# Kernel tuning notes

Measured on AMD Instinct MI355X. Metric: run time of the kernel, lower is better.

## Reference

```python
import jax, jax.numpy as jnp
import numpy as np

N = 100000      # nodes
E = 1600000     # edges
F_IN = 128      # num_features
H = 64          # hidden_channels
EPS = 1e-5      # batchnorm eps


def _bn(x, gamma, beta, mean, var):
    # inference-mode BatchNorm1d
    return (x - mean) * jax.lax.rsqrt(var + EPS) * gamma + beta


def setup_inputs() -> dict:
    key = jax.random.key(0)
    ks = jax.random.split(key, 16)

    def lin_w(k, fan_in, fan_out):
        return (jax.random.normal(k, (fan_in, fan_out), jnp.float32)
                * (1.0 / np.sqrt(fan_in)))

    return {
        "x": jax.random.normal(ks[0], (N, F_IN), jnp.float32),
        "edge_index": jax.random.randint(ks[1], (2, E), 0, N, dtype=jnp.int32),
        # node_encoder: Linear(F_IN,H) + BN
        "enc_W": lin_w(ks[2], F_IN, H), "enc_b": jnp.zeros((H,), jnp.float32),
        "enc_g": jnp.ones((H,), jnp.float32), "enc_beta": jnp.zeros((H,), jnp.float32),
        "enc_mean": jnp.zeros((H,), jnp.float32), "enc_var": jnp.ones((H,), jnp.float32),
        # GCNConv layers (PyG: lin without bias, bias added after aggregation)
        "conv1_W": lin_w(ks[3], H, H), "conv1_b": jnp.zeros((H,), jnp.float32),
        "conv2_W": lin_w(ks[4], H, H), "conv2_b": jnp.zeros((H,), jnp.float32),
        # edge_predictor: Linear(2H,H) + BN + Linear(H,1)
        "ep1_W": lin_w(ks[5], 2 * H, H), "ep1_b": jnp.zeros((H,), jnp.float32),
        "ep_g": jnp.ones((H,), jnp.float32), "ep_beta": jnp.zeros((H,), jnp.float32),
        "ep_mean": jnp.zeros((H,), jnp.float32), "ep_var": jnp.ones((H,), jnp.float32),
        "ep2_W": lin_w(ks[6], H, 1), "ep2_b": jnp.zeros((1,), jnp.float32),
    }


def reference(x, edge_index, enc_W, enc_b, enc_g, enc_beta, enc_mean, enc_var,
              conv1_W, conv1_b, conv2_W, conv2_b,
              ep1_W, ep1_b, ep_g, ep_beta, ep_mean, ep_var, ep2_W, ep2_b):
    row, col = edge_index[0], edge_index[1]

    # GCN normalization with added self-loops (symmetric D^-1/2 (A+I) D^-1/2)
    loops = jnp.arange(N, dtype=row.dtype)
    row_sl = jnp.concatenate([row, loops])          # [E+N]
    col_sl = jnp.concatenate([col, loops])
    deg = jax.ops.segment_sum(jnp.ones_like(col_sl, jnp.float32), col_sl, N)
    dinv = jnp.where(deg > 0, jax.lax.rsqrt(jnp.maximum(deg, 1.0)), 0.0)
    norm = dinv[row_sl] * dinv[col_sl]              # [E+N]

    def gcn_conv(h, W, b):
        hw = h @ W                                   # [N,H]
        msg = hw[row_sl] * norm[:, None]             # gather-scale  [E+N,H]
        return jax.ops.segment_sum(msg, col_sl, N) + b  # scatter-add

    # node encoder (inference: dropout = identity)
    h = jax.nn.relu(_bn(x @ enc_W + enc_b, enc_g, enc_beta, enc_mean, enc_var))
    h = jax.nn.relu(gcn_conv(h, conv1_W, conv1_b))
    h = jax.nn.relu(gcn_conv(h, conv2_W, conv2_b))
    node_embeddings = h

    # edge predictor: gather + cat + MLP + sigmoid
    ef = jnp.concatenate([h[row], h[col]], axis=1)   # [E, 2H]
    e = jax.nn.relu(_bn(ef @ ep1_W + ep1_b, ep_g, ep_beta, ep_mean, ep_var))
    edge_pred = jax.nn.sigmoid(e @ ep2_W + ep2_b)    # [E, 1]
    return node_embeddings, edge_pred
```

## Files before the change

### kernel.cpp

```cpp
#include <hip/hip_runtime.h>
#include <hip/hip_bf16.h>
#include <hip/hip_fp16.h>

#define NN 100000
#define NE 1600000
#define FIN 128
#define HD 64
#define NB_MF 1563
#define BSH 8
#define BUCK 256
#define NBUCK 392
#define BCAP 5120
#define CHUNK 4096
#define NCHUNK 391
#define ESPLIT 2
#define NEB (NBUCK*ESPLIT)
#define NFB 6250
#define NAGG 6250

typedef unsigned int uint32;
typedef _Float16 half8 __attribute__((ext_vector_type(8)));
typedef float f32x4 __attribute__((ext_vector_type(4)));
typedef float f32x8 __attribute__((ext_vector_type(8)));

__global__ void __launch_bounds__(256) k_prep(const float* __restrict__ encW, const float* __restrict__ c1W,
                                              const float* __restrict__ c2W, const float* __restrict__ ep1W,
                                              _Float16* __restrict__ wt,
                                              const float* __restrict__ encB, const float* __restrict__ encG,
                                              const float* __restrict__ encBe, const float* __restrict__ encM,
                                              const float* __restrict__ encV,
                                              const float* __restrict__ ep1b, const float* __restrict__ epG,
                                              const float* __restrict__ epBe, const float* __restrict__ epM,
                                              const float* __restrict__ epV,
                                              float* __restrict__ foldEnc, float* __restrict__ foldPre,
                                              int* __restrict__ bcnt, _Float16* __restrict__ bufBzero){
    int blk = blockIdx.x, t = threadIdx.x;
    if(blk < 96){
        int i = blk*256 + t;
        if(i < 8192){
            int n = i >> 7, k = i & 127;
            wt[i] = (_Float16)encW[k*64 + n];
        } else if(i < 12288){
            int j = i - 8192; int n = j >> 6, k = j & 63;
            wt[i] = (_Float16)c1W[k*64 + n];
        } else if(i < 16384){
            int j = i - 12288; int n = j >> 6, k = j & 63;
            wt[i] = (_Float16)c2W[k*64 + n];
        } else {
            int j = i - 16384; int h = j >> 12; int jj = j & 4095;
            int n = jj >> 6, k = jj & 63;
            wt[i] = (_Float16)ep1W[(h*64 + k)*64 + n];
        }
    } else {
        if(t < 64){
            int j = t;
            float s = encG[j]*rsqrtf(encV[j]+1e-5f);
            foldEnc[j]      = s;
            foldEnc[64+j]   = (encB[j]-encM[j])*s + encBe[j];
            float sp = epG[j]*rsqrtf(epV[j]+1e-5f);
            foldPre[j]      = sp;
            foldPre[64+j]   = sp;
            foldPre[128+j]  = sp*(ep1b[j]-epM[j]) + epBe[j];
            foldPre[192+j]  = 0.f;
            bufBzero[j]     = (_Float16)0.f;
        }
        for(int i = t; i < NBUCK; i += 256) bcnt[i] = 0;
    }
}

__global__ void __launch_bounds__(256) k_part(const int* __restrict__ row,
                                              const int* __restrict__ col,
                                              int* __restrict__ bcnt,
                                              uint32* __restrict__ staged,
                                              uint32* __restrict__ posE){
    __shared__ int h[512];
    __shared__ int sc[512];
    __shared__ int gb[512];
    __shared__ uint32 lcsr[CHUNK];
    __shared__ int dst[CHUNK];
    int t = threadIdx.x;
    int e0 = blockIdx.x * CHUNK;
    int e1 = min(e0 + CHUNK, NE);
    h[t] = 0; h[256+t] = 0;
    __syncthreads();
    for(int e = e0 + t; e < e1; e += 256)
        atomicAdd(&h[col[e] >> BSH], 1);
    __syncthreads();
    int c0 = h[t], c1 = h[256+t];
    int i2 = 256 + t;
    gb[t]  = (c0 > 0) ? atomicAdd(&bcnt[t], c0) : 0;
    gb[i2] = (i2 < NBUCK && c1 > 0) ? atomicAdd(&bcnt[i2], c1) : 0;
    sc[t] = c0; __syncthreads();
    for(int off = 1; off < 256; off <<= 1){
        int a = (t >= off) ? sc[t-off] : 0;
        __syncthreads();
        sc[t] += a;
        __syncthreads();
    }
    int sum0 = sc[255];
    __syncthreads();
    sc[i2] = c1; __syncthreads();
    for(int off = 1; off < 256; off <<= 1){
        int a = (t >= off) ? sc[i2-off] : 0;
        __syncthreads();
        sc[i2] += a;
        __syncthreads();
    }
    __syncthreads();
    {
        int st0 = sc[t] - c0;
        int st1 = sc[i2] + sum0 - c1;
        h[t]   = st0;
        h[i2]  = st1;
        sc[t]  = t*BCAP  + gb[t]  - st0;
        sc[i2] = i2*BCAP + gb[i2] - st1;
    }
    __syncthreads();
    for(int e = e0 + t; e < e1; e += 256){
        int c = col[e], r = row[e];
        int b = c >> BSH;
        int p = atomicAdd(&h[b], 1);
        lcsr[p] = ((uint32)r << BSH) | (uint32)(c & (BUCK-1));
        int slot = sc[b] + p;
        int off  = slot - b*BCAP;
        bool ok  = (off < BCAP);
        dst[p]   = ok ? slot : -1;
        posE[e]  = ok ? (uint32)slot : 0xFFFFFFFFu;
    }
    __syncthreads();
    int cnt = e1 - e0;
    for(int i = t; i < cnt; i += 256){
        int d = dst[i];
        if(d >= 0) staged[d] = lcsr[i];
    }
}

__global__ void __launch_bounds__(256) k_fill3(const int* __restrict__ bcnt,
                                               const uint32* __restrict__ staged,
                                               int* __restrict__ deg,
                                               int* __restrict__ starts,
                                               float* __restrict__ dinv,
                                               int* __restrict__ csr){
    __shared__ int h[BUCK];
    __shared__ int sc[BUCK];
    __shared__ int red[256];
    __shared__ int lcsr[BCAP];
    int b = blockIdx.x, t = threadIdx.x;
    int part = 0;
    for(int i = t; i < b; i += 256) part += min(bcnt[i], BCAP);
    red[t] = part; __syncthreads();
    for(int off = 128; off > 0; off >>= 1){
        if(t < off) red[t] += red[t+off];
        __syncthreads();
    }
    int base = red[0];
    h[t] = 0;
    __syncthreads();
    int cnt = min(bcnt[b], BCAP);
    const uint32* st = staged + (size_t)b*BCAP;
    for(int i = t; i < cnt; i += 256) atomicAdd(&h[st[i] & (BUCK-1)], 1);
    __syncthreads();
    int v = h[t];
    sc[t] = v; __syncthreads();
    for(int off = 1; off < 256; off <<= 1){
        int a = (t >= off) ? sc[t-off] : 0;
        __syncthreads();
        sc[t] += a;
        __syncthreads();
    }
    int ex = sc[t] - v;
    int n = b*BUCK + t;
    if(n < NN){
        deg[n]    = v;
        starts[n] = base + ex;
        dinv[n]   = rsqrtf((float)(v + 1));
    }
    h[t] = ex;
    __syncthreads();
    for(int i = t; i < cnt; i += 256){
        uint32 u = st[i];
        int p = atomicAdd(&h[u & (BUCK-1)], 1);
        lcsr[p] = (int)(u >> BSH);
    }
    __syncthreads();
    for(int i = t; i < cnt; i += 256) csr[base + i] = lcsr[i];
}

template<int K, bool AF32, bool FOLD, bool RELU, bool SCALE, int OS>
__global__ void __launch_bounds__(256) k_mfma(const void* __restrict__ Ain,
                                              const _Float16* __restrict__ Bt,
                                              const float* __restrict__ fold,
                                              const float* __restrict__ rowscale,
                                              _Float16* __restrict__ outh){
    constexpr int PS = K + 8;
    __shared__ _Float16 As[64*PS];
    __shared__ _Float16 Bs[64*PS];
    int t = threadIdx.x;
    int m0 = blockIdx.x*64;
    int jh = blockIdx.y;
    {
        const _Float16* src = Bt + (size_t)jh*64*K;
        for(int idx = t; idx < 64*(K/8); idx += 256){
            int n = idx/(K/8), c = idx%(K/8);
            *(half8*)&Bs[n*PS + c*8] = *(const half8*)&src[n*K + c*8];
        }
    }
    if(AF32){
        const float* A = (const float*)Ain;
        for(int idx = t; idx < 64*(K/4); idx += 256){
            int r = idx/(K/4), c = idx%(K/4);
            int rowi = m0 + r; if(rowi >= NN) rowi = NN-1;
            float4 v = *(const float4*)&A[(size_t)rowi*K + c*4];
            _Float16* d = &As[r*PS + c*4];
            d[0]=(_Float16)v.x; d[1]=(_Float16)v.y; d[2]=(_Float16)v.z; d[3]=(_Float16)v.w;
        }
    } else {
        const _Float16* A = (const _Float16*)Ain;
        for(int idx = t; idx < 64*(K/8); idx += 256){
            int r = idx/(K/8), c = idx%(K/8);
            int rowi = m0 + r; if(rowi >= NN) rowi = NN-1;
            *(half8*)&As[r*PS + c*8] = *(const half8*)&A[(size_t)rowi*K + c*8];
        }
    }
    __syncthreads();
    int w = t>>6, l = t&63;
    int lm = l&15, q = l>>4;
    f32x4 acc0 = {0.f,0.f,0.f,0.f}, acc1 = {0.f,0.f,0.f,0.f};
    f32x4 acc2 = {0.f,0.f,0.f,0.f}, acc3 = {0.f,0.f,0.f,0.f};
    const _Float16* arow = &As[(w*16+lm)*PS + q*8];
    const _Float16* brow = &Bs[lm*PS + q*8];
    #pragma unroll
    for(int ks = 0; ks < K/32; ks++){
        half8 a  = *(const half8*)(arow + ks*32);
        half8 b0 = *(const half8*)(brow + ks*32);
        half8 b1 = *(const half8*)(brow + 16*PS + ks*32);
        half8 b2 = *(const half8*)(brow + 32*PS + ks*32);
        half8 b3 = *(const half8*)(brow + 48*PS + ks*32);
        acc0 = __builtin_amdgcn_mfma_f32_16x16x32_f16(a, b0, acc0, 0,0,0);
        acc1 = __builtin_amdgcn_mfma_f32_16x16x32_f16(a, b1, acc1, 0,0,0);
        acc2 = __builtin_amdgcn_mfma_f32_16x16x32_f16(a, b2, acc2, 0,0,0);
        acc3 = __builtin_amdgcn_mfma_f32_16x16x32_f16(a, b3, acc3, 0,0,0);
    }
    f32x4 accs[4] = {acc0, acc1, acc2, acc3};
    #pragma unroll
    for(int nt = 0; nt < 4; nt++){
        int col = nt*16 + lm;
        int jcol = jh*64 + col;
        float fs = FOLD ? fold[jcol] : 0.f;
        float fb = FOLD ? fold[OS + jcol] : 0.f;
        #pragma unroll
        for(int r = 0; r < 4; r++){
            int rowi = m0 + w*16 + q*4 + r;
            if(rowi >= NN) continue;
            float v = accs[nt][r];
            if(FOLD) v = v*fs + fb;
            if(RELU) v = fmaxf(v, 0.f);
            if(SCALE) v *= rowscale[rowi];
            outh[(size_t)rowi*OS + jcol] = (_Float16)v;
        }
    }
}

__global__ void __launch_bounds__(256) k_agg4(const _Float16* __restrict__ hb,
                                              const int* __restrict__ starts,
                                              const int* __restrict__ deg,
                                              const int* __restrict__ csr,
                                              const float* __restrict__ dinv,
                                              const float* __restrict__ bias,
                                              _Float16* __restrict__ outh,
                                              float* __restrict__ outf){
    int t = threadIdx.x, w = t>>6, f = t&63;
    int n0 = blockIdx.x*16 + w*4;
    int s0 = __builtin_amdgcn_readfirstlane(starts[n0+0]);
    int s1 = __builtin_amdgcn_readfirstlane(starts[n0+1]);
    int s2 = __builtin_amdgcn_readfirstlane(starts[n0+2]);
    int s3 = __builtin_amdgcn_readfirstlane(starts[n0+3]);
    int d0 = __builtin_amdgcn_readfirstlane(deg[n0+0]);
    int d1 = __builtin_amdgcn_readfirstlane(deg[n0+1]);
    int d2 = __builtin_amdgcn_readfirstlane(deg[n0+2]);
    int d3 = __builtin_amdgcn_readfirstlane(deg[n0+3]);
    float a0 = 0.f, a1 = 0.f, a2 = 0.f, a3 = 0.f;
    int dmax = max(max(d0,d1), max(d2,d3));
    for(int i0 = 0; i0 < dmax; i0 += 64){
        int li0 = (i0+f < d0) ? csr[s0+i0+f] : NN;
        int li1 = (i0+f < d1) ? csr[s1+i0+f] : NN;
        int li2 = (i0+f < d2) ? csr[s2+i0+f] : NN;
        int li3 = (i0+f < d3) ? csr[s3+i0+f] : NN;
        int mm = min(dmax - i0, 64);
        for(int j = 0; j < mm; j += 8){
            float t0 = 0.f, t1 = 0.f, t2 = 0.f, t3 = 0.f;
            #pragma unroll
            for(int u = 0; u < 8; u++){
                int r0 = __builtin_amdgcn_readlane(li0, j+u);
                int r1 = __builtin_amdgcn_readlane(li1, j+u);
                int r2 = __builtin_amdgcn_readlane(li2, j+u);
                int r3 = __builtin_amdgcn_readlane(li3, j+u);
                t0 += (float)hb[(size_t)r0*64 + f];
                t1 += (float)hb[(size_t)r1*64 + f];
                t2 += (float)hb[(size_t)r2*64 + f];
                t3 += (float)hb[(size_t)r3*64 + f];
            }
            a0 += t0; a1 += t1; a2 += t2; a3 += t3;
        }
    }
    float bv = bias[f];
    float dn0 = dinv[n0+0], dn1 = dinv[n0+1], dn2 = dinv[n0+2], dn3 = dinv[n0+3];
    float sf0 = (float)hb[(size_t)(n0+0)*64 + f];
    float sf1 = (float)hb[(size_t)(n0+1)*64 + f];
    float sf2 = (float)hb[(size_t)(n0+2)*64 + f];
    float sf3 = (float)hb[(size_t)(n0+3)*64 + f];
    float o0 = fmaxf((a0 + sf0)*dn0 + bv, 0.f);
    float o1 = fmaxf((a1 + sf1)*dn1 + bv, 0.f);
    float o2 = fmaxf((a2 + sf2)*dn2 + bv, 0.f);
    float o3 = fmaxf((a3 + sf3)*dn3 + bv, 0.f);
    outh[(size_t)(n0+0)*64 + f] = (_Float16)o0;
    outh[(size_t)(n0+1)*64 + f] = (_Float16)o1;
    outh[(size_t)(n0+2)*64 + f] = (_Float16)o2;
    outh[(size_t)(n0+3)*64 + f] = (_Float16)o3;
    if(outf){
        outf[(size_t)(n0+0)*64 + f] = o0;
        outf[(size_t)(n0+1)*64 + f] = o1;
        outf[(size_t)(n0+2)*64 + f] = o2;
        outf[(size_t)(n0+3)*64 + f] = o3;
    }
}

__global__ void __launch_bounds__(512) k_edgeb(const int* __restrict__ bcnt,
                                               const uint32* __restrict__ staged,
                                               const _Float16* __restrict__ pre,
                                               const float* __restrict__ w2,
                                               const float* __restrict__ b2,
                                               _Float16* __restrict__ zqh){
    __shared__ half8 Bl[BUCK*8];
    int t = threadIdx.x;
    int item = ((int)blockIdx.x & 7)*98 + ((int)blockIdx.x >> 3);
    int b = item >> 1, s = item & 1;
    const _Float16* ps = pre;
    for(int idx = t; idx < BUCK*8; idx += 512){
        int rl = idx >> 3, ch = idx & 7;
        int n = (b << BSH) + rl; if(n >= NN) n = NN-1;
        Bl[rl*8 + (ch ^ (rl & 7))] = *(const half8*)(ps + (size_t)n*128 + 64 + ch*8);
    }
    __syncthreads();

    int cnt = min(bcnt[b], BCAP);
    int lo = (cnt * s) >> 1, hi = (cnt * (s+1)) >> 1;
    const uint32* st = staged + (size_t)b*BCAP;
    _Float16* zb = zqh + (size_t)b*BCAP;
    int p  = t & 7;
    int oc = t >> 3;
    f32x8 w2v = *(const f32x8*)(w2 + 8*p);
    float b2v = b2[0];

    auto edot = [&](uint32 u)->float{
        int r  = (int)(u >> BSH);
        int cl = (int)(u & (BUCK-1));
        half8 av = *(const half8*)(ps + (size_t)r*128 + 8*p);
        half8 bv = Bl[cl*8 + (p ^ (cl & 7))];
        half8 sv = av + bv;
        half8 zero8 = {};
        half8 rv = __builtin_elementwise_max(sv, zero8);
        f32x8 fv = __builtin_convertvector(rv, f32x8);
        float z;
        z  = fv[0]*w2v[0] + fv[1]*w2v[1];
        z  = fmaf(fv[2], w2v[2], z); z = fmaf(fv[3], w2v[3], z);
        z  = fmaf(fv[4], w2v[4], z); z = fmaf(fv[5], w2v[5], z);
        z  = fmaf(fv[6], w2v[6], z); z = fmaf(fv[7], w2v[7], z);
        return z;
    };

    int i = lo + oc;
    for(; i + 64 < hi; i += 128){
        uint32 u0 = st[i], u1 = st[i+64];
        float z0 = edot(u0);
        float z1 = edot(u1);
        z0 += __shfl_xor(z0, 1, 64); z1 += __shfl_xor(z1, 1, 64);
        z0 += __shfl_xor(z0, 2, 64); z1 += __shfl_xor(z1, 2, 64);
        z0 += __shfl_xor(z0, 4, 64); z1 += __shfl_xor(z1, 4, 64);
        if(p == 0){
            zb[i]    = (_Float16)(1.f/(1.f+__expf(-(z0+b2v))));
            zb[i+64] = (_Float16)(1.f/(1.f+__expf(-(z1+b2v))));
        }
    }
    for(; i < hi; i += 64){
        uint32 u0 = st[i];
        float z0 = edot(u0);
        z0 += __shfl_xor(z0, 1, 64);
        z0 += __shfl_xor(z0, 2, 64);
        z0 += __shfl_xor(z0, 4, 64);
        if(p == 0) zb[i] = (_Float16)(1.f/(1.f+__expf(-(z0+b2v))));
    }
}

__global__ void __launch_bounds__(256) k_final(const uint32* __restrict__ posE,
                                               const _Float16* __restrict__ zqh,
                                               float* __restrict__ out){
    int e = blockIdx.x*256 + threadIdx.x;
    if(e < NE){
        uint32 pz = posE[e];
        out[e] = (float)zqh[pz < (uint32)(NBUCK*BCAP) ? pz : 0u];
    }
}


extern "C" void kernel_launch(void* const* d_in, const int* in_sizes, int n_in,
                              void* d_out, int out_size, void* d_ws, size_t ws_size,
                              hipStream_t stream){
    const float* x   = (const float*)d_in[0];
    const int* ei    = (const int*)d_in[1];
    const int* row   = ei;
    const int* col   = ei + NE;
    const float* encW = (const float*)d_in[2],  *encB = (const float*)d_in[3];
    const float* encG = (const float*)d_in[4],  *encBe= (const float*)d_in[5];
    const float* encM = (const float*)d_in[6],  *encV = (const float*)d_in[7];
    const float* c1W  = (const float*)d_in[8],  *c1b  = (const float*)d_in[9];
    const float* c2W  = (const float*)d_in[10], *c2b  = (const float*)d_in[11];
    const float* ep1W = (const float*)d_in[12], *ep1b = (const float*)d_in[13];
    const float* epG  = (const float*)d_in[14], *epBe = (const float*)d_in[15];
    const float* epM  = (const float*)d_in[16], *epV  = (const float*)d_in[17];
    const float* ep2W = (const float*)d_in[18], *ep2b = (const float*)d_in[19];

    char* wsc = (char*)d_ws;
    size_t o = 0;
    auto alloc = [&](size_t bytes)->void*{
        void* p = wsc + o; o += (bytes + 255) & ~(size_t)255; return p;
    };
    int*      deg     = (int*)     alloc((size_t)NN*4);
    int*      starts  = (int*)     alloc((size_t)NN*4);
    int*      bcnt    = (int*)     alloc((size_t)NBUCK*4);
    int*      csr     = (int*)     alloc((size_t)NE*4);
    uint32*   staged  = (uint32*)  alloc((size_t)NBUCK*BCAP*4);
    float*    dinv    = (float*)   alloc((size_t)NN*4);
    float*    foldEnc = (float*)   alloc(128*4);
    float*    foldPre = (float*)   alloc(256*4);
    _Float16* wt      = (_Float16*)alloc(24576*2);
    _Float16* bufA    = (_Float16*)alloc((size_t)NN*64*2);
    _Float16* bufB    = (_Float16*)alloc((size_t)(NN+1)*64*2);
    _Float16* preh    = (_Float16*)alloc((size_t)NN*128*2);
    uint32*   posE    = (uint32*)  alloc((size_t)NE*4);
    _Float16* zqh     = (_Float16*)alloc((size_t)NBUCK*BCAP*2);

    float* outp = (float*)d_out;
    float* node_out = outp;
    float* edge_out = outp + (size_t)NN*64;

    k_prep <<<97, 256, 0, stream>>>(encW, c1W, c2W, ep1W, wt,
                                    encB, encG, encBe, encM, encV,
                                    ep1b, epG, epBe, epM, epV,
                                    foldEnc, foldPre, bcnt, bufB + (size_t)NN*64);
    k_part <<<NCHUNK, 256, 0, stream>>>(row, col, bcnt, staged, posE);
    k_fill3<<<NBUCK,  256, 0, stream>>>(bcnt, staged, deg, starts, dinv, csr);

    k_mfma<128,true,true,true,false,64><<<dim3(NB_MF,1), 256, 0, stream>>>
        (x, wt, foldEnc, nullptr, bufA);

    k_mfma<64,false,false,false,true,64><<<dim3(NB_MF,1), 256, 0, stream>>>
        (bufA, wt + 8192, nullptr, dinv, bufB);
    k_agg4 <<<NAGG, 256, 0, stream>>>(bufB, starts, deg, csr, dinv, c1b,
                                      bufA, nullptr);

    k_mfma<64,false,false,false,true,64><<<dim3(NB_MF,1), 256, 0, stream>>>
        (bufA, wt + 12288, nullptr, dinv, bufB);
    k_agg4 <<<NAGG, 256, 0, stream>>>(bufB, starts, deg, csr, dinv, c2b,
                                      bufA, node_out);

    k_mfma<64,false,true,false,false,128><<<dim3(NB_MF,2), 256, 0, stream>>>
        (bufA, wt + 16384, foldPre, nullptr, preh);

    k_edgeb<<<NEB, 512, 0, stream>>>(bcnt, staged, (const _Float16*)preh, ep2W, ep2b, zqh);
    k_final<<<NFB, 256, 0, stream>>>(posE, zqh, edge_out);
}
```

Before: 326.6 us.

## Merge independent preprocessing kernels into combined launches with block-range dispatch

Weight conversion and BN folding now run in the same launch as edge partitioning, split by block index. The bucket counter is cleared with a memset. CSR fill and the encoder MFMA GEMM share a second launch, with a shared-memory union sized for the larger of the two branches. This cuts launch count and tail gaps between independent stages, at the cost of a larger shared allocation for the fill blocks, which may reduce occupancy.

```diff
diff --git a/kernel.cpp b/kernel.cpp
--- a/kernel.cpp
+++ b/kernel.cpp
@@ -23,167 +23,222 @@
 typedef float f32x4 __attribute__((ext_vector_type(4)));
 typedef float f32x8 __attribute__((ext_vector_type(8)));
 
-__global__ void __launch_bounds__(256) k_prep(const float* __restrict__ encW, const float* __restrict__ c1W,
-                                              const float* __restrict__ c2W, const float* __restrict__ ep1W,
-                                              _Float16* __restrict__ wt,
-                                              const float* __restrict__ encB, const float* __restrict__ encG,
-                                              const float* __restrict__ encBe, const float* __restrict__ encM,
-                                              const float* __restrict__ encV,
-                                              const float* __restrict__ ep1b, const float* __restrict__ epG,
-                                              const float* __restrict__ epBe, const float* __restrict__ epM,
-                                              const float* __restrict__ epV,
-                                              float* __restrict__ foldEnc, float* __restrict__ foldPre,
-                                              int* __restrict__ bcnt, _Float16* __restrict__ bufBzero){
+__global__ void __launch_bounds__(256) k_pp(const int* __restrict__ row,
+                                            const int* __restrict__ col,
+                                            int* __restrict__ bcnt,
+                                            uint32* __restrict__ staged,
+                                            uint32* __restrict__ posE,
+                                            const float* __restrict__ encW, const float* __restrict__ c1W,
+                                            const float* __restrict__ c2W, const float* __restrict__ ep1W,
+                                            _Float16* __restrict__ wt,
+                                            const float* __restrict__ encB, const float* __restrict__ encG,
+                                            const float* __restrict__ encBe, const float* __restrict__ encM,
+                                            const float* __restrict__ encV,
+                                            const float* __restrict__ ep1b, const float* __restrict__ epG,
+                                            const float* __restrict__ epBe, const float* __restrict__ epM,
+                                            const float* __restrict__ epV,
+                                            float* __restrict__ foldEnc, float* __restrict__ foldPre,
+                                            _Float16* __restrict__ bufBzero){
     int blk = blockIdx.x, t = threadIdx.x;
-    if(blk < 96){
-        int i = blk*256 + t;
-        if(i < 8192){
-            int n = i >> 7, k = i & 127;
-            wt[i] = (_Float16)encW[k*64 + n];
-        } else if(i < 12288){
-            int j = i - 8192; int n = j >> 6, k = j & 63;
-            wt[i] = (_Float16)c1W[k*64 + n];
-        } else if(i < 16384){
-            int j = i - 12288; int n = j >> 6, k = j & 63;
-            wt[i] = (_Float16)c2W[k*64 + n];
+    if(blk < NCHUNK){
+        __shared__ int h[512];
+        __shared__ int sc[512];
+        __shared__ int gb[512];
+        __shared__ uint32 lcsr[CHUNK];
+        __shared__ int dst[CHUNK];
+        int e0 = blk * CHUNK;
+        int e1 = min(e0 + CHUNK, NE);
+        h[t] = 0; h[256+t] = 0;
+        __syncthreads();
+        for(int e = e0 + t; e < e1; e += 256)
+            atomicAdd(&h[col[e] >> BSH], 1);
+        __syncthreads();
+        int c0 = h[t], c1 = h[256+t];
+        int i2 = 256 + t;
+        gb[t]  = (c0 > 0) ? atomicAdd(&bcnt[t], c0) : 0;
+        gb[i2] = (i2 < NBUCK && c1 > 0) ? atomicAdd(&bcnt[i2], c1) : 0;
+        sc[t] = c0; __syncthreads();
+        for(int off = 1; off < 256; off <<= 1){
+            int a = (t >= off) ? sc[t-off] : 0;
+            __syncthreads();
+            sc[t] += a;
+            __syncthreads();
+        }
+        int sum0 = sc[255];
+        __syncthreads();
+        sc[i2] = c1; __syncthreads();
+        for(int off = 1; off < 256; off <<= 1){
+            int a = (t >= off) ? sc[i2-off] : 0;
+            __syncthreads();
+            sc[i2] += a;
+            __syncthreads();
+        }
+        __syncthreads();
+        {
+            int st0 = sc[t] - c0;
+            int st1 = sc[i2] + sum0 - c1;
+            h[t]   = st0;
+            h[i2]  = st1;
+            sc[t]  = t*BCAP  + gb[t]  - st0;
+            sc[i2] = i2*BCAP + gb[i2] - st1;
+        }
+        __syncthreads();
+        for(int e = e0 + t; e < e1; e += 256){
+            int c = col[e], r = row[e];
+            int b = c >> BSH;
+            int p = atomicAdd(&h[b], 1);
+            lcsr[p] = ((uint32)r << BSH) | (uint32)(c & (BUCK-1));
+            int slot = sc[b] + p;
+            int off  = slot - b*BCAP;
+            bool ok  = (off < BCAP);
+            dst[p]   = ok ? slot : -1;
+            posE[e]  = ok ? (uint32)slot : 0xFFFFFFFFu;
+        }
+        __syncthreads();
+        int cnt = e1 - e0;
+        for(int i = t; i < cnt; i += 256){
+            int d = dst[i];
+            if(d >= 0) staged[d] = lcsr[i];
+        }
+    } else {
+        int pblk = blk - NCHUNK;
+        if(pblk < 96){
+            int i = pblk*256 + t;
+            if(i < 8192){
+                int n = i >> 7, k = i & 127;
+                wt[i] = (_Float16)encW[k*64 + n];
+            } else if(i < 12288){
+                int j = i - 8192; int n = j >> 6, k = j & 63;
+                wt[i] = (_Float16)c1W[k*64 + n];
+            } else if(i < 16384){
+                int j = i - 12288; int n = j >> 6, k = j & 63;
+                wt[i] = (_Float16)c2W[k*64 + n];
+            } else {
+                int j = i - 16384; int hh = j >> 12; int jj = j & 4095;
+                int n = jj >> 6, k = jj & 63;
+                wt[i] = (_Float16)ep1W[(hh*64 + k)*64 + n];
+            }
         } else {
-            int j = i - 16384; int h = j >> 12; int jj = j & 4095;
-            int n = jj >> 6, k = jj & 63;
-            wt[i] = (_Float16)ep1W[(h*64 + k)*64 + n];
-        }
+            if(t < 64){
+                int j = t;
+                float s = encG[j]*rsqrtf(encV[j]+1e-5f);
+                foldEnc[j]      = s;
+                foldEnc[64+j]   = (encB[j]-encM[j])*s + encBe[j];
+                float sp = epG[j]*rsqrtf(epV[j]+1e-5f);
+                foldPre[j]      = sp;
+                foldPre[64+j]   = sp;
+                foldPre[128+j]  = sp*(ep1b[j]-epM[j]) + epBe[j];
+                foldPre[192+j]  = 0.f;
+                bufBzero[j]     = (_Float16)0.f;
+            }
+        }
+    }
+}
+
+__global__ void __launch_bounds__(256) k_fe(const int* __restrict__ bcnt,
+                                            const uint32* __restrict__ staged,
+                                            int* __restrict__ deg,
+                                            int* __restrict__ starts,
+                                            float* __restrict__ dinv,
+                                            int* __restrict__ csr,
+                                            const float* __restrict__ x,
+                                            const _Float16* __restrict__ wt,
+                                            const float* __restrict__ foldEnc,
+                                            _Float16* __restrict__ bufA){
+    __shared__ union U {
+        struct { int h[BUCK]; int sc[BUCK]; int red[256]; int lcsr[BCAP]; } f;
+        struct { _Float16 As[64*136]; _Float16 Bs[64*136]; } m;
+    } sh;
+    int blk = blockIdx.x, t = threadIdx.x;
+    if(blk < NBUCK){
+        int b = blk;
+        int part = 0;
+        for(int i = t; i < b; i += 256) part += min(bcnt[i], BCAP);
+        sh.f.red[t] = part; __syncthreads();
+        for(int off = 128; off > 0; off >>= 1){
+            if(t < off) sh.f.red[t] += sh.f.red[t+off];
+            __syncthreads();
+        }
+        int base = sh.f.red[0];
+        sh.f.h[t] = 0;
+        __syncthreads();
+        int cnt = min(bcnt[b], BCAP);
+        const uint32* st = staged + (size_t)b*BCAP;
+        for(int i = t; i < cnt; i += 256) atomicAdd(&sh.f.h[st[i] & (BUCK-1)], 1);
+        __syncthreads();
+        int v = sh.f.h[t];
+        sh.f.sc[t] = v; __syncthreads();
+        for(int off = 1; off < 256; off <<= 1){
+            int a = (t >= off) ? sh.f.sc[t-off] : 0;
+            __syncthreads();
+            sh.f.sc[t] += a;
+            __syncthreads();
+        }
+        int ex = sh.f.sc[t] - v;
+        int n = b*BUCK + t;
+        if(n < NN){
+            deg[n]    = v;
+            starts[n] = base + ex;
+            dinv[n]   = rsqrtf((float)(v + 1));
+        }
+        sh.f.h[t] = ex;
+        __syncthreads();
+        for(int i = t; i < cnt; i += 256){
+            uint32 u = st[i];
+            int p = atomicAdd(&sh.f.h[u & (BUCK-1)], 1);
+            sh.f.lcsr[p] = (int)(u >> BSH);
+        }
+        __syncthreads();
+        for(int i = t; i < cnt; i += 256) csr[base + i] = sh.f.lcsr[i];
     } else {
-        if(t < 64){
-            int j = t;
-            float s = encG[j]*rsqrtf(encV[j]+1e-5f);
-            foldEnc[j]      = s;
-            foldEnc[64+j]   = (encB[j]-encM[j])*s + encBe[j];
-            float sp = epG[j]*rsqrtf(epV[j]+1e-5f);
-            foldPre[j]      = sp;
-            foldPre[64+j]   = sp;
-            foldPre[128+j]  = sp*(ep1b[j]-epM[j]) + epBe[j];
-            foldPre[192+j]  = 0.f;
-            bufBzero[j]     = (_Float16)0.f;
-        }
-        for(int i = t; i < NBUCK; i += 256) bcnt[i] = 0;
-    }
-}
-
-__global__ void __launch_bounds__(256) k_part(const int* __restrict__ row,
-                                              const int* __restrict__ col,
-                                              int* __restrict__ bcnt,
-                                              uint32* __restrict__ staged,
-                                              uint32* __restrict__ posE){
-    __shared__ int h[512];
-    __shared__ int sc[512];
-    __shared__ int gb[512];
-    __shared__ uint32 lcsr[CHUNK];
-    __shared__ int dst[CHUNK];
-    int t = threadIdx.x;
-    int e0 = blockIdx.x * CHUNK;
-    int e1 = min(e0 + CHUNK, NE);
-    h[t] = 0; h[256+t] = 0;
-    __syncthreads();
-    for(int e = e0 + t; e < e1; e += 256)
-        atomicAdd(&h[col[e] >> BSH], 1);
-    __syncthreads();
-    int c0 = h[t], c1 = h[256+t];
-    int i2 = 256 + t;
-    gb[t]  = (c0 > 0) ? atomicAdd(&bcnt[t], c0) : 0;
-    gb[i2] = (i2 < NBUCK && c1 > 0) ? atomicAdd(&bcnt[i2], c1) : 0;
-    sc[t] = c0; __syncthreads();
-    for(int off = 1; off < 256; off <<= 1){
-        int a = (t >= off) ? sc[t-off] : 0;
-        __syncthreads();
-        sc[t] += a;
-        __syncthreads();
-    }
-    int sum0 = sc[255];
-    __syncthreads();
-    sc[i2] = c1; __syncthreads();
-    for(int off = 1; off < 256; off <<= 1){
-        int a = (t >= off) ? sc[i2-off] : 0;
-        __syncthreads();
-        sc[i2] += a;
-        __syncthreads();
-    }
-    __syncthreads();
-    {
-        int st0 = sc[t] - c0;
-        int st1 = sc[i2] + sum0 - c1;
-        h[t]   = st0;
-        h[i2]  = st1;
-        sc[t]  = t*BCAP  + gb[t]  - st0;
-        sc[i2] = i2*BCAP + gb[i2] - st1;
-    }
-    __syncthreads();
-    for(int e = e0 + t; e < e1; e += 256){
-        int c = col[e], r = row[e];
-        int b = c >> BSH;
-        int p = atomicAdd(&h[b], 1);
-        lcsr[p] = ((uint32)r << BSH) | (uint32)(c & (BUCK-1));
-        int slot = sc[b] + p;
-        int off  = slot - b*BCAP;
-        bool ok  = (off < BCAP);
-        dst[p]   = ok ? slot : -1;
-        posE[e]  = ok ? (uint32)slot : 0xFFFFFFFFu;
-    }
-    __syncthreads();
-    int cnt = e1 - e0;
-    for(int i = t; i < cnt; i += 256){
-        int d = dst[i];
-        if(d >= 0) staged[d] = lcsr[i];
-    }
-}
-
-__global__ void __launch_bounds__(256) k_fill3(const int* __restrict__ bcnt,
-                                               const uint32* __restrict__ staged,
-                                               int* __restrict__ deg,
-                                               int* __restrict__ starts,
-                                               float* __restrict__ dinv,
-                                               int* __restrict__ csr){
-    __shared__ int h[BUCK];
-    __shared__ int sc[BUCK];
-    __shared__ int red[256];
-    __shared__ int lcsr[BCAP];
-    int b = blockIdx.x, t = threadIdx.x;
-    int part = 0;
-    for(int i = t; i < b; i += 256) part += min(bcnt[i], BCAP);
-    red[t] = part; __syncthreads();
-    for(int off = 128; off > 0; off >>= 1){
-        if(t < off) red[t] += red[t+off];
-        __syncthreads();
-    }
-    int base = red[0];
-    h[t] = 0;
-    __syncthreads();
-    int cnt = min(bcnt[b], BCAP);
-    const uint32* st = staged + (size_t)b*BCAP;
-    for(int i = t; i < cnt; i += 256) atomicAdd(&h[st[i] & (BUCK-1)], 1);
-    __syncthreads();
-    int v = h[t];
-    sc[t] = v; __syncthreads();
-    for(int off = 1; off < 256; off <<= 1){
-        int a = (t >= off) ? sc[t-off] : 0;
-        __syncthreads();
-        sc[t] += a;
-        __syncthreads();
-    }
-    int ex = sc[t] - v;
-    int n = b*BUCK + t;
-    if(n < NN){
-        deg[n]    = v;
-        starts[n] = base + ex;
-        dinv[n]   = rsqrtf((float)(v + 1));
-    }
-    h[t] = ex;
-    __syncthreads();
-    for(int i = t; i < cnt; i += 256){
-        uint32 u = st[i];
-        int p = atomicAdd(&h[u & (BUCK-1)], 1);
-        lcsr[p] = (int)(u >> BSH);
-    }
-    __syncthreads();
-    for(int i = t; i < cnt; i += 256) csr[base + i] = lcsr[i];
+        constexpr int K = FIN, PS = K + 8;
+        int m0 = (blk - NBUCK)*64;
+        for(int idx = t; idx < 64*(K/8); idx += 256){
+            int n = idx/(K/8), c = idx%(K/8);
+            *(half8*)&sh.m.Bs[n*PS + c*8] = *(const half8*)&wt[n*K + c*8];
+        }
+        for(int idx = t; idx < 64*(K/4); idx += 256){
+            int r = idx/(K/4), c = idx%(K/4);
+            int rowi = m0 + r; if(rowi >= NN) rowi = NN-1;
+            float4 v = *(const float4*)&x[(size_t)rowi*K + c*4];
+            _Float16* d = &sh.m.As[r*PS + c*4];
+            d[0]=(_Float16)v.x; d[1]=(_Float16)v.y; d[2]=(_Float16)v.z; d[3]=(_Float16)v.w;
+        }
+        __syncthreads();
+        int w = t>>6, l = t&63;
+        int lm = l&15, q = l>>4;
+        f32x4 acc0 = {0.f,0.f,0.f,0.f}, acc1 = {0.f,0.f,0.f,0.f};
+        f32x4 acc2 = {0.f,0.f,0.f,0.f}, acc3 = {0.f,0.f,0.f,0.f};
+        const _Float16* arow = &sh.m.As[(w*16+lm)*PS + q*8];
+        const _Float16* brow = &sh.m.Bs[lm*PS + q*8];
+        #pragma unroll
+        for(int ks = 0; ks < K/32; ks++){
+            half8 a  = *(const half8*)(arow + ks*32);
+            half8 b0 = *(const half8*)(brow + ks*32);
+            half8 b1 = *(const half8*)(brow + 16*PS + ks*32);
+            half8 b2 = *(const half8*)(brow + 32*PS + ks*32);
+            half8 b3 = *(const half8*)(brow + 48*PS + ks*32);
+            acc0 = __builtin_amdgcn_mfma_f32_16x16x32_f16(a, b0, acc0, 0,0,0);
+            acc1 = __builtin_amdgcn_mfma_f32_16x16x32_f16(a, b1, acc1, 0,0,0);
+            acc2 = __builtin_amdgcn_mfma_f32_16x16x32_f16(a, b2, acc2, 0,0,0);
+            acc3 = __builtin_amdgcn_mfma_f32_16x16x32_f16(a, b3, acc3, 0,0,0);
+        }
+        f32x4 accs[4] = {acc0, acc1, acc2, acc3};
+        #pragma unroll
+        for(int nt = 0; nt < 4; nt++){
+            int jcol = nt*16 + lm;
+            float fs = foldEnc[jcol];
+            float fb = foldEnc[64 + jcol];
+            #pragma unroll
+            for(int r = 0; r < 4; r++){
+                int rowi = m0 + w*16 + q*4 + r;
+                if(rowi >= NN) continue;
+                float v = accs[nt][r]*fs + fb;
+                v = fmaxf(v, 0.f);
+                bufA[(size_t)rowi*64 + jcol] = (_Float16)v;
+            }
+        }
+    }
 }
 
 template<int K, bool AF32, bool FOLD, bool RELU, bool SCALE, int OS>
@@ -444,15 +499,14 @@
     float* node_out = outp;
     float* edge_out = outp + (size_t)NN*64;
 
-    k_prep <<<97, 256, 0, stream>>>(encW, c1W, c2W, ep1W, wt,
-                                    encB, encG, encBe, encM, encV,
-                                    ep1b, epG, epBe, epM, epV,
-                                    foldEnc, foldPre, bcnt, bufB + (size_t)NN*64);
-    k_part <<<NCHUNK, 256, 0, stream>>>(row, col, bcnt, staged, posE);
-    k_fill3<<<NBUCK,  256, 0, stream>>>(bcnt, staged, deg, starts, dinv, csr);
-
-    k_mfma<128,true,true,true,false,64><<<dim3(NB_MF,1), 256, 0, stream>>>
-        (x, wt, foldEnc, nullptr, bufA);
+    hipMemsetAsync(bcnt, 0, (size_t)NBUCK*4, stream);
+    k_pp <<<NCHUNK + 97, 256, 0, stream>>>(row, col, bcnt, staged, posE,
+                                           encW, c1W, c2W, ep1W, wt,
+                                           encB, encG, encBe, encM, encV,
+                                           ep1b, epG, epBe, epM, epV,
+                                           foldEnc, foldPre, bufB + (size_t)NN*64);
+    k_fe <<<NBUCK + NB_MF, 256, 0, stream>>>(bcnt, staged, deg, starts, dinv, csr,
+                                             x, wt, foldEnc, bufA);
 
     k_mfma<64,false,false,false,true,64><<<dim3(NB_MF,1), 256, 0, stream>>>
         (bufA, wt + 8192, nullptr, dinv, bufB);
```

New measurement: 319.2 us (median of 2 runs). -2.3%, faster.
